# Kernel tuning notes

Hardware: AMD Instinct MI355X
Metric: run time of the kernel (lower is better)

The kernel has to match this reference:

```python
import jax, jax.numpy as jnp
import numpy as np

B, S, D, R, N = 4, 2048, 1024, 256, 16

def setup_inputs() -> dict:
    key = jax.random.key(0)
    k1, k2, k3, k4, k5 = jax.random.split(key, 5)
    return {
        "x": jax.random.normal(k1, (B, S, D), dtype=jnp.float32),
        "feature_know": jax.random.normal(k2, (N, D, R), dtype=jnp.float32) * 0.02,
        "restore_know": jax.random.normal(k3, (N, R, D), dtype=jnp.float32) * 0.02,
        "feature_know_w": jax.random.uniform(k4, (B, S, N), dtype=jnp.float32),
        "restore_know_w": jax.random.uniform(k5, (B, S, N), dtype=jnp.float32),
    }

def reference(x, feature_know, restore_know, feature_know_w, restore_know_w):
    # Feature stage: weighted mixture over N knowledge neurons, D -> R.
    # Same math as einsum('bsd,ndr->bsnr') then einsum('bsnr,bsn->bsr'),
    # fused so the [B,S,N,R] intermediate is reduced over N on the fly.
    h = jnp.einsum('bsd,ndr,bsn->bsr', x, feature_know, feature_know_w)
    # Restore stage: R -> D, again a weighted mixture over N neurons.
    out = jnp.einsum('bsr,nrd,bsn->bsd', h, restore_know, restore_know_w)
    # Dropout is evaluated deterministically (eval mode): identity.
    return out
```

## Files before the change

kernel.cpp:

```cpp
#include <hip/hip_runtime.h>

typedef unsigned short u16;
typedef unsigned int u32;
typedef __attribute__((ext_vector_type(4))) float f32x4;
typedef __attribute__((ext_vector_type(8))) short bf16x8;
typedef __attribute__((ext_vector_type(4))) unsigned short u16x4;

#define MFMA(a, b, c) __builtin_amdgcn_mfma_f32_16x16x32_bf16((a), (b), (c), 0, 0, 0)

static constexpr int M_TOK = 8192;

__device__ __forceinline__ u16 f2bf(float f) {
  u32 u = __float_as_uint(f);
  return (u16)((u + 0x7FFFu + ((u >> 16) & 1u)) >> 16);
}
__device__ __forceinline__ float bf2f(u16 b) {
  u32 u = ((u32)b) << 16;
  return __uint_as_float(u);
}
__device__ __forceinline__ void gload16(const u16* g, u16* l) {
  __builtin_amdgcn_global_load_lds(
      (const __attribute__((address_space(1))) u32*)(const void*)g,
      (__attribute__((address_space(3))) u32*)(void*)l, 16, 0, 0);
}

#define PH_BAR()                                     \
  do {                                               \
    __builtin_amdgcn_sched_barrier(0);               \
    __builtin_amdgcn_s_barrier();                    \
    asm volatile("s_waitcnt lgkmcnt(0)" ::: "memory"); \
    __builtin_amdgcn_sched_barrier(0);               \
  } while (0)
#define PH_END()                       \
  do {                                 \
    __builtin_amdgcn_sched_barrier(0); \
    __builtin_amdgcn_s_barrier();      \
  } while (0)

__global__ void cast_x_kernel(const float* __restrict__ in, u16* __restrict__ out, int total4) {
  for (int i = blockIdx.x * blockDim.x + threadIdx.x; i < total4; i += gridDim.x * blockDim.x) {
    float4 v = ((const float4*)in)[i];
    u16x4 o;
    o[0] = f2bf(v.x); o[1] = f2bf(v.y); o[2] = f2bf(v.z); o[3] = f2bf(v.w);
    ((u16x4*)out)[i] = o;
  }
}

__global__ void tcast_kernel(const float* __restrict__ in, u16* __restrict__ out, int P, int Q) {
  __shared__ float tile[32][33];
  const int z = blockIdx.z;
  const int q0 = blockIdx.x * 32, p0 = blockIdx.y * 32;
  const float* src = in + (size_t)z * P * Q;
  u16* dst = out + (size_t)z * P * Q;
  const int tx = threadIdx.x & 31, ty = threadIdx.x >> 5;
#pragma unroll
  for (int k = 0; k < 4; ++k)
    tile[ty + k * 8][tx] = src[(size_t)(p0 + ty + k * 8) * Q + q0 + tx];
  __syncthreads();
#pragma unroll
  for (int k = 0; k < 4; ++k)
    dst[(size_t)(q0 + ty + k * 8) * P + p0 + tx] = f2bf(tile[tx][ty + k * 8]);
}

__global__ void combine_h(const u16* __restrict__ T, const float* __restrict__ Wf,
                          u16* __restrict__ h) {
  const int m = blockIdx.x * 4 + (threadIdx.x >> 6);
  const int lane = threadIdx.x & 63;
  const u16* rowp = T + (size_t)m * 4096;
  float h0 = 0.f, h1 = 0.f, h2 = 0.f, h3 = 0.f;
#pragma unroll
  for (int n = 0; n < 16; ++n) {
    u16x4 v = *(const u16x4*)&rowp[n * 256 + lane * 4];
    const float wf = Wf[(size_t)m * 16 + n];
    h0 += wf * bf2f(v[0]); h1 += wf * bf2f(v[1]);
    h2 += wf * bf2f(v[2]); h3 += wf * bf2f(v[3]);
  }
  u16x4 o;
  o[0] = f2bf(h0); o[1] = f2bf(h1); o[2] = f2bf(h2); o[3] = f2bf(h3);
  *(u16x4*)&h[(size_t)m * 256 + lane * 4] = o;
}

template <int NT>
__global__ __launch_bounds__(512, 2) void gemm256(
    const u16* __restrict__ A, const u16* __restrict__ Bm, void* __restrict__ OutV,
    const int N, const int K) {
  constexpr int NITER = NT / 2;
  __shared__ u16 lds[65536];

  const int tid = threadIdx.x;
  const int lane = tid & 63;
  const int wid = tid >> 6;
  const int wr = wid >> 2, wc = wid & 3;

  const int L = blockIdx.y * gridDim.x + blockIdx.x;
  const int ordered = (L & 7) * 64 + (L >> 3);
  const int cid = ordered >> 5, win = ordered & 31;
  const int bx = (cid & 3) * 4 + (win & 3);
  const int by = (cid >> 2) * 8 + (win >> 2);
  const int m0 = by * 256, bn0 = bx * 256;

  const int arow = lane & 15;
  const int acol = (lane >> 4) * 16;
  const int sw = (arow & 7) << 4;
  const int lo0 = arow * 128 + (acol ^ sw);
  const int lo1 = arow * 128 + ((64 + acol) ^ sw);

  const u16* Abase = A + (size_t)m0 * K;
  const u16* Bbase = Bm + (size_t)bn0 * K;

  f32x4 acc[8][4];
#pragma unroll
  for (int i = 0; i < 8; ++i)
#pragma unroll
    for (int j = 0; j < 4; ++j) acc[i][j] = (f32x4){0.f, 0.f, 0.f, 0.f};

  auto STAGE = [&](int b, int isB, int hf, int kt) {
    const u16* G = isB ? Bbase : Abase;
    u16* Lp = &lds[isB * 32768 + (b * 2 + hf) * 8192];
#pragma unroll
    for (int j = 0; j < 2; ++j) {
      const int q = j * 8192 + tid * 16;
      const int grow = q >> 7;
      const int gcol = ((q & 127) ^ (((q >> 7) & 7) << 4)) >> 1;
      gload16(G + (size_t)(hf * 128 + grow) * K + kt * 64 + gcol,
              Lp + ((j * 8192 + wid * 1024) >> 1));
    }
  };
  auto LOAD_AV = [&](bf16x8 (&v)[4][2], int b, int mh) {
    const char* p = (const char*)lds + b * 32768 + (wr * 128 + mh * 64) * 128;
#pragma unroll
    for (int mi = 0; mi < 4; ++mi) {
      v[mi][0] = *(const bf16x8*)(p + mi * 2048 + lo0);
      v[mi][1] = *(const bf16x8*)(p + mi * 2048 + lo1);
    }
  };
  auto LOAD_BV = [&](bf16x8 (&v)[2][2], int b, int nq) {
#pragma unroll
    for (int nj = 0; nj < 2; ++nj) {
      const int rb = wc * 64 + (nq * 2 + nj) * 16;
      const char* p = (const char*)lds + 65536 + b * 32768 + rb * 128;
      v[nj][0] = *(const bf16x8*)(p + lo0);
      v[nj][1] = *(const bf16x8*)(p + lo1);
    }
  };

#define QUAD2(AV, BV0, BV1, MH)                                                \
  do {                                                                         \
    _Pragma("unroll") for (int ks = 0; ks < 2; ++ks) {                         \
      _Pragma("unroll") for (int mi = 0; mi < 4; ++mi) {                       \
        _Pragma("unroll") for (int nj = 0; nj < 2; ++nj) {                     \
          acc[(MH)*4 + mi][nj] = MFMA(AV[mi][ks], BV0[nj][ks], acc[(MH)*4 + mi][nj]); \
          acc[(MH)*4 + mi][2 + nj] = MFMA(AV[mi][ks], BV1[nj][ks], acc[(MH)*4 + mi][2 + nj]); \
        }                                                                      \
      }                                                                        \
    }                                                                          \
  } while (0)

  bf16x8 av[4][2], avh[4][2], bv0[2][2], bv1[2][2];

  STAGE(0, 0, 0, 0); STAGE(0, 0, 1, 0); STAGE(0, 1, 0, 0); STAGE(0, 1, 1, 0);
  STAGE(1, 1, 0, 1); STAGE(1, 0, 0, 1);
  asm volatile("s_waitcnt vmcnt(4)" ::: "memory");
  __builtin_amdgcn_sched_barrier(0);
  __builtin_amdgcn_s_barrier();

#pragma unroll 1
  for (int i = 0; i < NITER; ++i) {
    const int ta = 2 * i, tb = ta + 1;
    const bool st = (i + 1 < NITER);
    LOAD_AV(av, 0, 0); LOAD_BV(bv0, 0, 0); LOAD_BV(bv1, 0, 1);
    STAGE(1, 0, 1, tb); STAGE(1, 1, 1, tb);
    PH_BAR();
    __builtin_amdgcn_s_setprio(1);
    QUAD2(av, bv0, bv1, 0);
    __builtin_amdgcn_s_setprio(0);
    PH_END();
    LOAD_AV(avh, 0, 1);
    if (st) { STAGE(0, 1, 0, ta + 2); STAGE(0, 0, 0, ta + 2); }
    PH_BAR();
    __builtin_amdgcn_s_setprio(1);
    QUAD2(avh, bv0, bv1, 1);
    __builtin_amdgcn_s_setprio(0);
    if (st) asm volatile("s_waitcnt vmcnt(4)" ::: "memory");
    else    asm volatile("s_waitcnt vmcnt(0)" ::: "memory");
    PH_END();
    LOAD_AV(av, 1, 0); LOAD_BV(bv0, 1, 0); LOAD_BV(bv1, 1, 1);
    if (st) { STAGE(0, 0, 1, ta + 2); STAGE(0, 1, 1, ta + 2); }
    PH_BAR();
    __builtin_amdgcn_s_setprio(1);
    QUAD2(av, bv0, bv1, 0);
    __builtin_amdgcn_s_setprio(0);
    PH_END();
    LOAD_AV(avh, 1, 1);
    if (st) { STAGE(1, 1, 0, tb + 2); STAGE(1, 0, 0, tb + 2); }
    PH_BAR();
    __builtin_amdgcn_s_setprio(1);
    QUAD2(avh, bv0, bv1, 1);
    __builtin_amdgcn_s_setprio(0);
    if (st) asm volatile("s_waitcnt vmcnt(4)" ::: "memory");
    PH_END();
  }

#pragma unroll
  for (int MI = 0; MI < 8; ++MI) {
    const int r0 = wr * 128 + MI * 16 + (lane >> 4) * 4;
#pragma unroll
    for (int NJ = 0; NJ < 4; ++NJ) {
      const int c = wc * 64 + NJ * 16 + (lane & 15);
#pragma unroll
      for (int j = 0; j < 4; ++j) {
        const int rr = r0 + j;
        *(u16*)((char*)lds + ((rr * 512 + c * 2) ^ ((rr & 7) << 4))) = f2bf(acc[MI][NJ][j]);
      }
    }
  }
  __syncthreads();
#pragma unroll
  for (int i = 0; i < 16; ++i) {
    const int rr = wid * 32 + i * 2 + (lane >> 5);
    const int unit = lane & 31;
    bf16x8 v = *(const bf16x8*)((const char*)lds + ((rr * 512 + unit * 16) ^ ((rr & 7) << 4)));
    *(bf16x8*)((u16*)OutV + (size_t)(m0 + rr) * N + bn0 + unit * 8) = v;
  }
}
#undef QUAD2

__global__ __launch_bounds__(512, 2) void gemm_fold(
    const u16* __restrict__ A,
    const u16* __restrict__ Bn,
    const float* __restrict__ W,
    float* __restrict__ Out) {
  __shared__ u16 ldsB[8][8192];
  __shared__ u16 Wlds[16][264];

  const int tid = threadIdx.x;
  const int lane = tid & 63;
  const int wid = tid >> 6;
  const int kh = wid >> 2;
  const int wrM = (wid >> 1) & 1;
  const int wcN = wid & 1;

  const int L = blockIdx.y * gridDim.x + blockIdx.x;
  const int ordered = (L & 7) * 64 + (L >> 3);
  const int cid = ordered >> 5, win = ordered & 31;
  const int bx = (cid & 3) * 2 + (win & 1);
  const int by = (cid >> 2) * 16 + (win >> 1);
  const int m0 = by * 128, d0 = bx * 128;

  const int arow = lane & 15;
  const int acol = (lane >> 4) * 16;
  const int sw = (arow & 7) << 4;
  const int lo0 = arow * 128 + (acol ^ sw);
  const int lo1 = arow * 128 + ((64 + acol) ^ sw);

  for (int i = tid; i < 128 * 16; i += 512) {
    const int row = i >> 4, n = i & 15;
    Wlds[n][row] = f2bf(W[(size_t)(m0 + row) * 16 + n]);
  }

  auto ASTAGE = [&](int kt) {
    const u16* G = A + (size_t)m0 * 256;
    u16* Lp = &ldsB[kt][0];
#pragma unroll
    for (int j = 0; j < 2; ++j) {
      const int q = j * 8192 + tid * 16;
      const int grow = q >> 7;
      const int gcol = ((q & 127) ^ (((q >> 7) & 7) << 4)) >> 1;
      gload16(G + (size_t)grow * 256 + kt * 64 + gcol, Lp + ((j * 8192 + wid * 1024) >> 1));
    }
  };
  ASTAGE(0); ASTAGE(1); ASTAGE(2); ASTAGE(3);
  __syncthreads();
  bf16x8 avk[4][4];
#pragma unroll
  for (int c2 = 0; c2 < 2; ++c2) {
#pragma unroll
    for (int mi = 0; mi < 4; ++mi) {
      const char* p = (const char*)&ldsB[kh * 2 + c2][0] + (wrM * 64 + mi * 16) * 128;
      avk[c2 * 2 + 0][mi] = *(const bf16x8*)(p + lo0);
      avk[c2 * 2 + 1][mi] = *(const bf16x8*)(p + lo1);
    }
  }
  __syncthreads();

  auto BSTAGE = [&](int ss) {
    const int n = ss >> 1, h = ss & 1, p = ss & 3;
    const u16* G = Bn + ((size_t)n * 1024 + d0) * 256;
#pragma unroll
    for (int t = 0; t < 2; ++t) {
      u16* Lp = &ldsB[2 * p + t][0];
      const int kt = h + 2 * t;
#pragma unroll
      for (int j = 0; j < 2; ++j) {
        const int q = j * 8192 + tid * 16;
        const int grow = q >> 7;
        const int gcol = ((q & 127) ^ (((q >> 7) & 7) << 4)) >> 1;
        gload16(G + (size_t)grow * 256 + kt * 64 + gcol, Lp + ((j * 8192 + wid * 1024) >> 1));
      }
    }
  };

  f32x4 acc_t[4][4], acc_g[4][4];
#pragma unroll
  for (int mi = 0; mi < 4; ++mi)
#pragma unroll
    for (int nj = 0; nj < 4; ++nj) {
      acc_t[mi][nj] = (f32x4){0.f, 0.f, 0.f, 0.f};
      acc_g[mi][nj] = (f32x4){0.f, 0.f, 0.f, 0.f};
    }
  bf16x8 bv[4][2];

  BSTAGE(0); BSTAGE(1); BSTAGE(2);
  asm volatile("s_waitcnt vmcnt(8)" ::: "memory");
  __builtin_amdgcn_sched_barrier(0);
  __builtin_amdgcn_s_barrier();

  auto SSTEP = [&](int ss, int h, bool do_stage, int vmsel) {
    const int p = ss & 3;
    const char* pB = (const char*)&ldsB[2 * p + kh][0];
#pragma unroll
    for (int nj = 0; nj < 4; ++nj) {
      const char* q = pB + (wcN * 64 + nj * 16) * 128;
      bv[nj][0] = *(const bf16x8*)(q + lo0);
      bv[nj][1] = *(const bf16x8*)(q + lo1);
    }
    if (do_stage) BSTAGE(ss + 3);
    PH_BAR();
    __builtin_amdgcn_s_setprio(1);
#pragma unroll
    for (int ks = 0; ks < 2; ++ks)
#pragma unroll
      for (int mi = 0; mi < 4; ++mi)
#pragma unroll
        for (int nj = 0; nj < 4; ++nj)
          acc_g[mi][nj] = MFMA(avk[2 * h + ks][mi], bv[nj][ks], acc_g[mi][nj]);
    __builtin_amdgcn_s_setprio(0);
    if (vmsel == 8)      asm volatile("s_waitcnt vmcnt(8)" ::: "memory");
    else if (vmsel == 4) asm volatile("s_waitcnt vmcnt(4)" ::: "memory");
    else if (vmsel == 0) asm volatile("s_waitcnt vmcnt(0)" ::: "memory");
    PH_END();
  };
  auto FOLD = [&](int n) {
#pragma unroll
    for (int mi = 0; mi < 4; ++mi) {
      const int rbase = wrM * 64 + mi * 16 + (lane >> 4) * 4;
      u16x4 wq = *(const u16x4*)&Wlds[n][rbase];
      const float w0 = bf2f(wq[0]), w1 = bf2f(wq[1]), w2 = bf2f(wq[2]), w3 = bf2f(wq[3]);
#pragma unroll
      for (int nj = 0; nj < 4; ++nj) {
        acc_t[mi][nj][0] += w0 * acc_g[mi][nj][0];
        acc_t[mi][nj][1] += w1 * acc_g[mi][nj][1];
        acc_t[mi][nj][2] += w2 * acc_g[mi][nj][2];
        acc_t[mi][nj][3] += w3 * acc_g[mi][nj][3];
        acc_g[mi][nj] = (f32x4){0.f, 0.f, 0.f, 0.f};
      }
    }
  };

#pragma unroll 1
  for (int nn = 0; nn < 14; ++nn) {
    SSTEP(nn * 2 + 0, 0, true, 8);
    SSTEP(nn * 2 + 1, 1, true, 8);
    FOLD(nn);
  }
  SSTEP(28, 0, true, 8);
  SSTEP(29, 1, false, 4);
  FOLD(14);
  SSTEP(30, 0, false, 0);
  SSTEP(31, 1, false, -1);
  FOLD(15);

  __syncthreads();
  char* red = (char*)&ldsB[0][0];
  auto rb = [&](int r, int c) { return (r * 512 + c * 4) ^ ((r & 7) << 4); };
  if (kh == 1) {
#pragma unroll
    for (int mi = 0; mi < 4; ++mi)
#pragma unroll
      for (int j = 0; j < 4; ++j) {
        const int r = wrM * 64 + mi * 16 + (lane >> 4) * 4 + j;
#pragma unroll
        for (int nj = 0; nj < 4; ++nj)
          *(float*)(red + rb(r, wcN * 64 + nj * 16 + (lane & 15))) = acc_t[mi][nj][j];
      }
  }
  __syncthreads();
  if (kh == 0) {
#pragma unroll
    for (int mi = 0; mi < 4; ++mi)
#pragma unroll
      for (int j = 0; j < 4; ++j) {
        const int r = wrM * 64 + mi * 16 + (lane >> 4) * 4 + j;
#pragma unroll
        for (int nj = 0; nj < 4; ++nj) {
          float* p = (float*)(red + rb(r, wcN * 64 + nj * 16 + (lane & 15)));
          *p += acc_t[mi][nj][j];
        }
      }
  }
  __syncthreads();
#pragma unroll
  for (int i = 0; i < 8; ++i) {
    const int r = wid * 16 + i * 2 + (lane >> 5);
    const int unit = lane & 31;
    f32x4 v = *(const f32x4*)(red + ((r * 512 + unit * 16) ^ ((r & 7) << 4)));
    *(f32x4*)(Out + (size_t)(m0 + r) * 1024 + d0 + unit * 4) = v;
  }
}

extern "C" void kernel_launch(void* const* d_in, const int* in_sizes, int n_in,
                              void* d_out, int out_size, void* d_ws, size_t ws_size,
                              hipStream_t stream) {
  const float* x  = (const float*)d_in[0];
  const float* F  = (const float*)d_in[1];
  const float* Rk = (const float*)d_in[2];
  const float* Wf = (const float*)d_in[3];
  const float* Wr = (const float*)d_in[4];
  float* out = (float*)d_out;

  char* ws = (char*)d_ws;
  u16* X16 = (u16*)(ws);
  u16* B1  = (u16*)(ws + (16u << 20));
  u16* Rt  = (u16*)(ws + (24u << 20));
  u16* T   = (u16*)(ws + (32u << 20));
  u16* h16 = (u16*)(ws);

  cast_x_kernel<<<2048, 256, 0, stream>>>(x, X16, (M_TOK * 1024) / 4);
  tcast_kernel<<<dim3(8, 32, 16), 256, 0, stream>>>(F, B1, 1024, 256);
  tcast_kernel<<<dim3(32, 8, 16), 256, 0, stream>>>(Rk, Rt, 256, 1024);

  gemm256<16><<<dim3(16, 32, 1), 512, 0, stream>>>(X16, B1, T, 4096, 1024);
  combine_h<<<2048, 256, 0, stream>>>(T, Wf, h16);
  gemm_fold<<<dim3(8, 64, 1), 512, 0, stream>>>(h16, Rt, Wr, out);
}
```

Baseline: 174.8 us.

## Double-buffer per-neuron accumulators to overlap weighted fold with MFMA

Splits the per-neuron GEMM accumulator into two ping-pong register sets so the weighted fold of one neuron's partial product runs interleaved with the MFMAs of the next neuron. Each fold is cut into halves spread across phases, weight loads are prefetched from LDS earlier, and the first MFMA of each group starts from zero instead of explicitly clearing the accumulators. The aim is to remove the serial fold bubble between neurons, at the cost of 64 more accumulator registers, which may lower occupancy or cause spills.

```diff
diff --git a/kernel.cpp b/kernel.cpp
--- a/kernel.cpp
+++ b/kernel.cpp
@@ -300,75 +300,107 @@
     }
   };
 
-  f32x4 acc_t[4][4], acc_g[4][4];
+  f32x4 acc_t[4][4], gA[4][4], gB[4][4];
 #pragma unroll
   for (int mi = 0; mi < 4; ++mi)
 #pragma unroll
+    for (int nj = 0; nj < 4; ++nj) acc_t[mi][nj] = (f32x4){0.f, 0.f, 0.f, 0.f};
+  const f32x4 vz = {0.f, 0.f, 0.f, 0.f};
+  bf16x8 bv[4][2];
+  u16x4 wpf[4];
+
+  auto BVLOAD = [&](int p) {
+    const char* pB = (const char*)&ldsB[2 * p + kh][0];
+#pragma unroll
     for (int nj = 0; nj < 4; ++nj) {
-      acc_t[mi][nj] = (f32x4){0.f, 0.f, 0.f, 0.f};
-      acc_g[mi][nj] = (f32x4){0.f, 0.f, 0.f, 0.f};
-    }
-  bf16x8 bv[4][2];
+      const char* q = pB + (wcN * 64 + nj * 16) * 128;
+      bv[nj][0] = *(const bf16x8*)(q + lo0);
+      bv[nj][1] = *(const bf16x8*)(q + lo1);
+    }
+  };
+  auto WPFL = [&](int n) {
+#pragma unroll
+    for (int mi = 0; mi < 4; ++mi)
+      wpf[mi] = *(const u16x4*)&Wlds[n][wrM * 64 + mi * 16 + (lane >> 4) * 4];
+  };
+
+#define MFMA_GRP(G, H, FIRST)                                                  \
+  do {                                                                         \
+    _Pragma("unroll") for (int ks = 0; ks < 2; ++ks) {                         \
+      _Pragma("unroll") for (int mi = 0; mi < 4; ++mi) {                       \
+        _Pragma("unroll") for (int nj = 0; nj < 4; ++nj) {                     \
+          G[mi][nj] = MFMA(avk[2 * (H) + ks][mi], bv[nj][ks],                  \
+                           ((FIRST) && ks == 0) ? vz : G[mi][nj]);             \
+        }                                                                      \
+      }                                                                        \
+    }                                                                          \
+  } while (0)
+
+#define FOLD_HALF(F, HB)                                                       \
+  do {                                                                         \
+    _Pragma("unroll") for (int mi = 2 * (HB); mi < 2 * (HB) + 2; ++mi) {       \
+      const float w0 = bf2f(wpf[mi][0]), w1 = bf2f(wpf[mi][1]),                \
+                  w2 = bf2f(wpf[mi][2]), w3 = bf2f(wpf[mi][3]);                \
+      _Pragma("unroll") for (int nj = 0; nj < 4; ++nj) {                       \
+        acc_t[mi][nj][0] += w0 * F[mi][nj][0];                                 \
+        acc_t[mi][nj][1] += w1 * F[mi][nj][1];                                 \
+        acc_t[mi][nj][2] += w2 * F[mi][nj][2];                                 \
+        acc_t[mi][nj][3] += w3 * F[mi][nj][3];                                 \
+      }                                                                        \
+    }                                                                          \
+  } while (0)
 
   BSTAGE(0); BSTAGE(1); BSTAGE(2);
   asm volatile("s_waitcnt vmcnt(8)" ::: "memory");
   __builtin_amdgcn_sched_barrier(0);
   __builtin_amdgcn_s_barrier();
 
-  auto SSTEP = [&](int ss, int h, bool do_stage, int vmsel) {
-    const int p = ss & 3;
-    const char* pB = (const char*)&ldsB[2 * p + kh][0];
-#pragma unroll
-    for (int nj = 0; nj < 4; ++nj) {
-      const char* q = pB + (wcN * 64 + nj * 16) * 128;
-      bv[nj][0] = *(const bf16x8*)(q + lo0);
-      bv[nj][1] = *(const bf16x8*)(q + lo1);
-    }
-    if (do_stage) BSTAGE(ss + 3);
-    PH_BAR();
-    __builtin_amdgcn_s_setprio(1);
-#pragma unroll
-    for (int ks = 0; ks < 2; ++ks)
-#pragma unroll
-      for (int mi = 0; mi < 4; ++mi)
-#pragma unroll
-        for (int nj = 0; nj < 4; ++nj)
-          acc_g[mi][nj] = MFMA(avk[2 * h + ks][mi], bv[nj][ks], acc_g[mi][nj]);
-    __builtin_amdgcn_s_setprio(0);
-    if (vmsel == 8)      asm volatile("s_waitcnt vmcnt(8)" ::: "memory");
-    else if (vmsel == 4) asm volatile("s_waitcnt vmcnt(4)" ::: "memory");
-    else if (vmsel == 0) asm volatile("s_waitcnt vmcnt(0)" ::: "memory");
-    PH_END();
-  };
-  auto FOLD = [&](int n) {
-#pragma unroll
-    for (int mi = 0; mi < 4; ++mi) {
-      const int rbase = wrM * 64 + mi * 16 + (lane >> 4) * 4;
-      u16x4 wq = *(const u16x4*)&Wlds[n][rbase];
-      const float w0 = bf2f(wq[0]), w1 = bf2f(wq[1]), w2 = bf2f(wq[2]), w3 = bf2f(wq[3]);
-#pragma unroll
-      for (int nj = 0; nj < 4; ++nj) {
-        acc_t[mi][nj][0] += w0 * acc_g[mi][nj][0];
-        acc_t[mi][nj][1] += w1 * acc_g[mi][nj][1];
-        acc_t[mi][nj][2] += w2 * acc_g[mi][nj][2];
-        acc_t[mi][nj][3] += w3 * acc_g[mi][nj][3];
-        acc_g[mi][nj] = (f32x4){0.f, 0.f, 0.f, 0.f};
-      }
-    }
-  };
-
 #pragma unroll 1
-  for (int nn = 0; nn < 14; ++nn) {
-    SSTEP(nn * 2 + 0, 0, true, 8);
-    SSTEP(nn * 2 + 1, 1, true, 8);
-    FOLD(nn);
-  }
-  SSTEP(28, 0, true, 8);
-  SSTEP(29, 1, false, 4);
-  FOLD(14);
-  SSTEP(30, 0, false, 0);
-  SSTEP(31, 1, false, -1);
-  FOLD(15);
+  for (int np = 0; np < 8; ++np) {
+    const int s0 = 4 * np;
+    const bool last = (np == 7);
+    BVLOAD(0); if (np) WPFL(2 * np - 1); BSTAGE(s0 + 3);
+    PH_BAR();
+    __builtin_amdgcn_s_setprio(1);
+    if (np) FOLD_HALF(gB, 0);
+    MFMA_GRP(gA, 0, true);
+    __builtin_amdgcn_s_setprio(0);
+    asm volatile("s_waitcnt vmcnt(8)" ::: "memory");
+    PH_END();
+    BVLOAD(1); if (!last) BSTAGE(s0 + 4);
+    PH_BAR();
+    __builtin_amdgcn_s_setprio(1);
+    if (np) FOLD_HALF(gB, 1);
+    MFMA_GRP(gA, 1, false);
+    __builtin_amdgcn_s_setprio(0);
+    if (!last) asm volatile("s_waitcnt vmcnt(8)" ::: "memory");
+    else       asm volatile("s_waitcnt vmcnt(4)" ::: "memory");
+    PH_END();
+    BVLOAD(2); WPFL(2 * np); if (!last) BSTAGE(s0 + 5);
+    PH_BAR();
+    __builtin_amdgcn_s_setprio(1);
+    FOLD_HALF(gA, 0);
+    MFMA_GRP(gB, 0, true);
+    __builtin_amdgcn_s_setprio(0);
+    if (!last) asm volatile("s_waitcnt vmcnt(8)" ::: "memory");
+    else       asm volatile("s_waitcnt vmcnt(0)" ::: "memory");
+    PH_END();
+    BVLOAD(3); if (!last) BSTAGE(s0 + 6);
+    PH_BAR();
+    __builtin_amdgcn_s_setprio(1);
+    FOLD_HALF(gA, 1);
+    MFMA_GRP(gB, 1, false);
+    __builtin_amdgcn_s_setprio(0);
+    if (!last) asm volatile("s_waitcnt vmcnt(8)" ::: "memory");
+    PH_END();
+  }
+  WPFL(15);
+  asm volatile("s_waitcnt lgkmcnt(0)" ::: "memory");
+  __builtin_amdgcn_sched_barrier(0);
+  FOLD_HALF(gB, 0);
+  FOLD_HALF(gB, 1);
+#undef MFMA_GRP
+#undef FOLD_HALF
 
   __syncthreads();
   char* red = (char*)&ldsB[0][0];
```

After: 369.9 us. 2.12x slower.
